# Kernel optimization log

Measured on AMD Instinct MI355X. Metric: run time of the kernel, lower is better.

## Reference

```python
import jax, jax.numpy as jnp
import numpy as np

NEG = -9e15

def _gat_layer(x, adj, W, a_src, a_dst):
    # x: [B,N,Fin], W: [Fin,Fout], a_src/a_dst: [Fout], adj: [N,N]
    h = jnp.einsum('bnf,fo->bno', x, W)                    # [B,N,Fout]
    e_src = jnp.einsum('bno,o->bn', h, a_src)              # [B,N]
    e_dst = jnp.einsum('bno,o->bn', h, a_dst)              # [B,N]
    e = jax.nn.leaky_relu(e_src[:, :, None] + e_dst[:, None, :], 0.2)  # [B,N,N]
    att = jax.nn.softmax(jnp.where(adj > 0, e, NEG), axis=-1)
    return jnp.einsum('bij,bjo->bio', att, h)              # [B,N,Fout]

def setup_inputs() -> dict:
    key = jax.random.key(0)
    ks = jax.random.split(key, 12)
    B, N, Fin = 8, 2048, 128
    H = [128, 128, 64]
    C = 128
    s = lambda *d: 1.0 / np.sqrt(d[0])
    inp = {
        'x':   jax.random.normal(ks[0], (B, N, Fin), jnp.float32),
        'adj': jax.random.normal(ks[1], (N, N), jnp.float32),
        'W1':  jax.random.normal(ks[2], (Fin, H[0]), jnp.float32) * s(Fin),
        'a1s': jax.random.normal(ks[3], (H[0],), jnp.float32) * s(H[0]),
        'a1d': jax.random.normal(ks[4], (H[0],), jnp.float32) * s(H[0]),
        'W2':  jax.random.normal(ks[5], (H[0], H[1]), jnp.float32) * s(H[0]),
        'a2s': jax.random.normal(ks[6], (H[1],), jnp.float32) * s(H[1]),
        'a2d': jax.random.normal(ks[7], (H[1],), jnp.float32) * s(H[1]),
        'W3':  jax.random.normal(ks[8], (H[1], H[2]), jnp.float32) * s(H[1]),
        'a3s': jax.random.normal(ks[9], (H[2],), jnp.float32) * s(H[2]),
        'a3d': jax.random.normal(ks[10], (H[2],), jnp.float32) * s(H[2]),
        'Wlin': jax.random.normal(ks[11], (H[2] * N, C), jnp.float32) * s(H[2] * N),
        'blin': jnp.zeros((C,), jnp.float32),
    }
    return inp

def reference(x, adj, W1, a1s, a1d, W2, a2s, a2d, W3, a3s, a3d, Wlin, blin):
    out = jax.nn.relu(_gat_layer(x, adj, W1, a1s, a1d))
    out = jax.nn.relu(_gat_layer(out, adj, W2, a2s, a2d))
    out = jax.nn.relu(_gat_layer(out, adj, W3, a3s, a3d))
    B = out.shape[0]
    out = out.reshape(B, -1)              # flatten [B, N*H3]
    return out @ Wlin + blin              # [B, num_classes]
```

## Files before the change

### kernel.cpp

```cpp
#include <hip/hip_runtime.h>
#include <stdint.h>


typedef unsigned short u16;
typedef __bf16 bf16x8 __attribute__((ext_vector_type(8)));
typedef float f32x4 __attribute__((ext_vector_type(4)));
typedef float f32x2 __attribute__((ext_vector_type(2)));
typedef u16 u16x8 __attribute__((ext_vector_type(8)));
typedef u16 u16x4 __attribute__((ext_vector_type(4)));

#define LOG2E 1.44269504088896340736f

__device__ __forceinline__ float b2f(u16 u) {
    union { unsigned int i; float f; } v; v.i = ((unsigned int)u) << 16; return v.f;
}
__device__ __forceinline__ u16 f2b(float f) {
    union { float f; unsigned int i; } v; v.f = f;
    unsigned int i = v.i;
    return (u16)((i + 0x7fffu + ((i >> 16) & 1u)) >> 16);
}
__device__ __forceinline__ float fast_exp2(float x) {
#if __has_builtin(__builtin_amdgcn_exp2f)
    return __builtin_amdgcn_exp2f(x);
#else
    return exp2f(x);
#endif
}

union ABfrag { bf16x8 v; u16x8 u; };

__global__ void __launch_bounds__(256) k_mask(const float* __restrict__ adj,
                                              uint32_t* __restrict__ adjm) {
    const int w = threadIdx.x >> 6, lane = threadIdx.x & 63;
    const int row = blockIdx.x * 4 + w;
    const float* ar = adj + (size_t)row * 2048;
    uint32_t* mr = adjm + (size_t)row * 64;
    for (int j0 = 0; j0 < 2048; j0 += 64) {
        unsigned long long m = __ballot(ar[j0 + lane] > 0.f);
        if (lane == 0) {
            mr[(j0 >> 5)] = (uint32_t)m;
            mr[(j0 >> 5) + 1] = (uint32_t)(m >> 32);
        }
    }
}

__global__ void k_prep(const float* __restrict__ W1, const float* __restrict__ W2,
                       const float* __restrict__ W3,
                       const float* __restrict__ a1s, const float* __restrict__ a1d,
                       const float* __restrict__ a2s, const float* __restrict__ a2d,
                       const float* __restrict__ a3s, const float* __restrict__ a3d,
                       u16* __restrict__ Wt1, u16* __restrict__ Wt2, u16* __restrict__ Wt3,
                       float* __restrict__ u1s, float* __restrict__ u1d,
                       float* __restrict__ u2s, float* __restrict__ u2d,
                       float* __restrict__ u3s, float* __restrict__ u3d) {
    if (blockIdx.x == 160) {
        int f = threadIdx.x;
        if (f < 128) {
            float s1 = 0.f, d1 = 0.f, s2 = 0.f, d2 = 0.f, s3 = 0.f, d3 = 0.f;
            for (int o = 0; o < 128; ++o) { float w = W1[f * 128 + o]; s1 += w * a1s[o]; d1 += w * a1d[o]; }
            for (int o = 0; o < 128; ++o) { float w = W2[f * 128 + o]; s2 += w * a2s[o]; d2 += w * a2d[o]; }
            for (int o = 0; o <  64; ++o) { float w = W3[f *  64 + o]; s3 += w * a3s[o]; d3 += w * a3d[o]; }
            u1s[f] = s1 * LOG2E; u1d[f] = d1 * LOG2E;
            u2s[f] = s2 * LOG2E; u2d[f] = d2 * LOG2E;
            u3s[f] = s3 * LOG2E; u3d[f] = d3 * LOG2E;
        }
        return;
    }
    int idx = blockIdx.x * 256 + threadIdx.x;
    if (idx < 16384) {
        int f = idx >> 7, o = idx & 127;
        Wt1[o * 128 + f] = f2b(W1[idx]);
    } else if (idx < 32768) {
        int j = idx - 16384; int f = j >> 7, o = j & 127;
        Wt2[o * 128 + f] = f2b(W2[j]);
    } else if (idx < 40960) {
        int j = idx - 32768; int f = j >> 6, o = j & 63;
        Wt3[o * 128 + f] = f2b(W3[j]);
    }
}

template <int F, bool XF32>
__global__ void __launch_bounds__(256) k_h(const void* __restrict__ xv,
                                           const u16* __restrict__ Wt,
                                           const float* __restrict__ us,
                                           const float* __restrict__ ud,
                                           u16* __restrict__ h_t,
                                           float* __restrict__ esf,
                                           float* __restrict__ edf) {
    constexpr int NTB = F / 32;
    constexpr int TNP = 72;
    __shared__ __align__(16) u16 hl[(F / 2) * TNP];

    const int b = blockIdx.x;
    const int nb2 = blockIdx.y;
    const int nblk = nb2 >> 1, ohalf = nb2 & 1;
    const int tid = threadIdx.x;
    const int w = tid >> 6, lane = tid & 63;
    const int quad = lane >> 4, l15 = lane & 15;
    const int n0w = nblk * 64 + w * 16;
    const int i_a = n0w + l15;

    ABfrag afr[4];
    float ps = 0.f, pd = 0.f;
    if (XF32) {
        const float* xr = (const float*)xv + ((size_t)(b * 2048 + i_a)) * 128;
#pragma unroll
        for (int kk = 0; kk < 4; ++kk) {
            const int o8 = kk * 32 + quad * 8;
            float4 x0 = *reinterpret_cast<const float4*>(xr + o8);
            float4 x1 = *reinterpret_cast<const float4*>(xr + o8 + 4);
            float4 s0 = *reinterpret_cast<const float4*>(us + o8);
            float4 s1 = *reinterpret_cast<const float4*>(us + o8 + 4);
            float4 d0 = *reinterpret_cast<const float4*>(ud + o8);
            float4 d1 = *reinterpret_cast<const float4*>(ud + o8 + 4);
            ps += x0.x * s0.x + x0.y * s0.y + x0.z * s0.z + x0.w * s0.w
                + x1.x * s1.x + x1.y * s1.y + x1.z * s1.z + x1.w * s1.w;
            pd += x0.x * d0.x + x0.y * d0.y + x0.z * d0.z + x0.w * d0.w
                + x1.x * d1.x + x1.y * d1.y + x1.z * d1.z + x1.w * d1.w;
            afr[kk].u[0] = f2b(x0.x); afr[kk].u[1] = f2b(x0.y);
            afr[kk].u[2] = f2b(x0.z); afr[kk].u[3] = f2b(x0.w);
            afr[kk].u[4] = f2b(x1.x); afr[kk].u[5] = f2b(x1.y);
            afr[kk].u[6] = f2b(x1.z); afr[kk].u[7] = f2b(x1.w);
        }
    } else {
        const u16* xr = (const u16*)xv + ((size_t)(b * 2048 + i_a)) * 128;
#pragma unroll
        for (int kk = 0; kk < 4; ++kk) {
            const int o8 = kk * 32 + quad * 8;
            u16x8 xa = *reinterpret_cast<const u16x8*>(xr + o8);
            afr[kk].u = xa;
            float4 s0 = *reinterpret_cast<const float4*>(us + o8);
            float4 s1 = *reinterpret_cast<const float4*>(us + o8 + 4);
            float4 d0 = *reinterpret_cast<const float4*>(ud + o8);
            float4 d1 = *reinterpret_cast<const float4*>(ud + o8 + 4);
            float xf[8];
#pragma unroll
            for (int j = 0; j < 8; ++j) xf[j] = b2f(xa[j]);
            ps += xf[0] * s0.x + xf[1] * s0.y + xf[2] * s0.z + xf[3] * s0.w
                + xf[4] * s1.x + xf[5] * s1.y + xf[6] * s1.z + xf[7] * s1.w;
            pd += xf[0] * d0.x + xf[1] * d0.y + xf[2] * d0.z + xf[3] * d0.w
                + xf[4] * d1.x + xf[5] * d1.y + xf[6] * d1.z + xf[7] * d1.w;
        }
    }
    if (ohalf == 0) {
        ps += __shfl_xor(ps, 16, 64); ps += __shfl_xor(ps, 32, 64);
        pd += __shfl_xor(pd, 16, 64); pd += __shfl_xor(pd, 32, 64);
        if (quad == 0) {
            float2 sv; sv.x = fast_exp2(ps); sv.y = fast_exp2(0.2f * ps);
            *reinterpret_cast<float2*>(esf + (size_t)(b * 2048 + i_a) * 2) = sv;
            edf[(size_t)b * 4096 + i_a]        = fast_exp2(pd);
            edf[(size_t)b * 4096 + 2048 + i_a] = fast_exp2(0.2f * pd);
        }
    }

    f32x4 acc[NTB];
#pragma unroll
    for (int nt = 0; nt < NTB; ++nt) acc[nt] = (f32x4){0.f, 0.f, 0.f, 0.f};
#pragma unroll
    for (int kk = 0; kk < 4; ++kk) {
#pragma unroll
        for (int nt = 0; nt < NTB; ++nt) {
            bf16x8 bfv = *reinterpret_cast<const bf16x8*>(
                Wt + (ohalf * (F / 2) + nt * 16 + l15) * 128 + kk * 32 + quad * 8);
            acc[nt] = __builtin_amdgcn_mfma_f32_16x16x32_bf16(afr[kk].v, bfv, acc[nt], 0, 0, 0);
        }
    }

#pragma unroll
    for (int nt = 0; nt < NTB; ++nt)
#pragma unroll
        for (int r = 0; r < 4; ++r)
            hl[(nt * 16 + l15) * TNP + w * 16 + quad * 4 + r] = f2b(acc[nt][r]);
    __syncthreads();
    if (tid < F) {
        int o_loc = tid >> 1, half32 = tid & 1;
        const u16* src = hl + o_loc * TNP + half32 * 32;
        u16* dst = h_t + ((size_t)(b * F + ohalf * (F / 2) + o_loc)) * 2048
                   + nblk * 64 + half32 * 32;
#pragma unroll
        for (int c = 0; c < 4; ++c)
            *reinterpret_cast<u16x8*>(dst + c * 8) =
                *reinterpret_cast<const u16x8*>(src + c * 8);
    }
}

template <int F, bool OUT_F32>
__global__ void __launch_bounds__(256, 4) k_attn(const float* __restrict__ esf,
                                                 const float* __restrict__ edf,
                                                 const uint32_t* __restrict__ adjm,
                                                 const u16* __restrict__ h_t,
                                                 void* __restrict__ outp) {
    constexpr int FH  = F / 2;
    constexpr int NT2 = FH / 16;
    constexpr int LP_BYTES = 8192 + 8192 + 8192;
    constexpr int CB_BYTES = 4 * 32 * FH * 4 + 512;
    constexpr int LDS_BYTES = (LP_BYTES > CB_BYTES) ? LP_BYTES : CB_BYTES;
    __shared__ __align__(16) char Sraw[LDS_BYTES];
    float* EdL = (float*)Sraw;
    float* FdL = (float*)(Sraw + 8192);
    uint32_t* mL = (uint32_t*)(Sraw + 16384);
    float* part = (float*)Sraw;
    float* denp = (float*)(Sraw + 4 * 32 * FH * 4);

    const int b = blockIdx.x;
    const int i0 = blockIdx.y * 32;
    const int ch = blockIdx.z;
    const int c0 = ch * FH;
    const int tid = threadIdx.x;
    const int w = tid >> 6;
    const int lane = tid & 63;
    const int quad = lane >> 4, l15 = lane & 15;
    const int r0 = l15, r1 = l15 + 16;

    const float2 e0p = *reinterpret_cast<const float2*>(esf + ((size_t)(b * 2048 + i0 + r0)) * 2);
    const float2 e1p = *reinterpret_cast<const float2*>(esf + ((size_t)(b * 2048 + i0 + r1)) * 2);
    const float Es0 = e0p.x, Fs0 = e0p.y, Es1 = e1p.x, Fs1 = e1p.y;
    const u16* hb = h_t + (size_t)b * F * 2048;

    ABfrag onesf;
#pragma unroll
    for (int j = 0; j < 8; ++j) onesf.u[j] = 0x3F80;

    f32x4 acc0[NT2], acc1[NT2];
#pragma unroll
    for (int nt = 0; nt < NT2; ++nt) {
        acc0[nt] = (f32x4){0.f, 0.f, 0.f, 0.f};
        acc1[nt] = (f32x4){0.f, 0.f, 0.f, 0.f};
    }
    f32x4 dn0 = (f32x4){0.f, 0.f, 0.f, 0.f};
    f32x4 dn1 = (f32x4){0.f, 0.f, 0.f, 0.f};

    {
        const float4* eds = (const float4*)(edf + (size_t)b * 4096);
        const float4* fds = (const float4*)(edf + (size_t)b * 4096 + 2048);
        float4* edd = (float4*)EdL;
        float4* fdd = (float4*)FdL;
#pragma unroll
        for (int t = 0; t < 2; ++t) {
            edd[tid + t * 256] = eds[tid + t * 256];
            fdd[tid + t * 256] = fds[tid + t * 256];
        }
        const uint2* msrc = (const uint2*)(adjm + (size_t)i0 * 64);
#pragma unroll
        for (int t = 0; t < 4; ++t) {
            int idx = tid + t * 256;
            int r = idx >> 5, k2 = idx & 31;
            uint2 v = msrc[idx];
            mL[r * 64 + ((2 * k2) ^ r)] = v.x;
            mL[r * 64 + ((2 * k2 + 1) ^ r)] = v.y;
        }
    }
    __syncthreads();

    const int jbase = w * 16;
    auto loadB = [&](int t, ABfrag* bt) {
        const size_t coff = (size_t)((jbase + t) * 32 + quad * 8);
#pragma unroll
        for (int nt = 0; nt < NT2; ++nt)
            bt[nt].u = *reinterpret_cast<const u16x8*>(
                hb + (size_t)(c0 + nt * 16 + l15) * 2048 + coff);
    };

    auto computeTile = [&](int t, ABfrag* bt) {
        const int jt = jbase + t;
        const int j0 = jt * 32;
        const uint32_t mm0 = mL[r0 * 64 + (jt ^ r0)] >> (quad * 8);
        const uint32_t mm1 = mL[r1 * 64 + (jt ^ r1)] >> (quad * 8);
        const f32x2* edp = (const f32x2*)(EdL + j0 + quad * 8);
        const f32x2* fdp = (const f32x2*)(FdL + j0 + quad * 8);

        ABfrag af0, af1;
#pragma unroll
        for (int p = 0; p < 4; ++p) {
            const f32x2 ed = edp[p];
            const f32x2 fd = fdp[p];
            f32x2 a0 = ed * Es0, b0 = fd * Fs0;
            f32x2 a1 = ed * Es1, b1 = fd * Fs1;
            float w0x = fmaxf(a0.x, b0.x), w0y = fmaxf(a0.y, b0.y);
            float w1x = fmaxf(a1.x, b1.x), w1y = fmaxf(a1.y, b1.y);
            const int s0x = ((int)(mm0 << (31 - (p * 2)))) >> 31;
            const int s0y = ((int)(mm0 << (31 - (p * 2 + 1)))) >> 31;
            const int s1x = ((int)(mm1 << (31 - (p * 2)))) >> 31;
            const int s1y = ((int)(mm1 << (31 - (p * 2 + 1)))) >> 31;
            w0x = __uint_as_float(__float_as_uint(w0x) & (uint32_t)s0x);
            w0y = __uint_as_float(__float_as_uint(w0y) & (uint32_t)s0y);
            w1x = __uint_as_float(__float_as_uint(w1x) & (uint32_t)s1x);
            w1y = __uint_as_float(__float_as_uint(w1y) & (uint32_t)s1y);
            af0.v[p * 2]     = (__bf16)w0x;
            af0.v[p * 2 + 1] = (__bf16)w0y;
            af1.v[p * 2]     = (__bf16)w1x;
            af1.v[p * 2 + 1] = (__bf16)w1y;
        }
        __builtin_amdgcn_s_setprio(1);
#pragma unroll
        for (int nt = 0; nt < NT2; ++nt) {
            acc0[nt] = __builtin_amdgcn_mfma_f32_16x16x32_bf16(af0.v, bt[nt].v, acc0[nt], 0, 0, 0);
            acc1[nt] = __builtin_amdgcn_mfma_f32_16x16x32_bf16(af1.v, bt[nt].v, acc1[nt], 0, 0, 0);
        }
        dn0 = __builtin_amdgcn_mfma_f32_16x16x32_bf16(af0.v, onesf.v, dn0, 0, 0, 0);
        dn1 = __builtin_amdgcn_mfma_f32_16x16x32_bf16(af1.v, onesf.v, dn1, 0, 0, 0);
        __builtin_amdgcn_s_setprio(0);
    };

    ABfrag btA[NT2], btB[NT2];
    loadB(0, btA);
    for (int t = 0; t < 16; t += 2) {
        loadB(t + 1, btB);
        computeTile(t, btA);
        if (t + 2 < 16) loadB(t + 2, btA);
        computeTile(t + 1, btB);
    }

    __syncthreads();
    {
        float* pw = part + (size_t)w * 32 * FH;
#pragma unroll
        for (int nt = 0; nt < NT2; ++nt)
#pragma unroll
            for (int r = 0; r < 4; ++r) {
                pw[(quad * 4 + r) * FH + nt * 16 + l15] = acc0[nt][r];
                pw[(16 + quad * 4 + r) * FH + nt * 16 + l15] = acc1[nt][r];
            }
#pragma unroll
        for (int r = 0; r < 4; ++r) {
            denp[w * 32 + quad * 4 + r] = dn0[r];
            denp[w * 32 + 16 + quad * 4 + r] = dn1[r];
        }
    }
    __syncthreads();
    {
        constexpr int C4 = FH / 4;
        for (int idx = tid; idx < 32 * C4; idx += 256) {
            const int row = idx / C4, c4 = idx % C4;
            f32x4 s = *reinterpret_cast<const f32x4*>(&part[row * FH + c4 * 4]);
#pragma unroll
            for (int ww = 1; ww < 4; ++ww)
                s += *reinterpret_cast<const f32x4*>(&part[(ww * 32 + row) * FH + c4 * 4]);
            const float den = denp[row] + denp[32 + row] + denp[64 + row] + denp[96 + row];
            const float dinv = 1.0f / fmaxf(den, 1e-30f);
            if (OUT_F32) {
                float4 o;
                o.x = fmaxf(s[0] * dinv, 0.f); o.y = fmaxf(s[1] * dinv, 0.f);
                o.z = fmaxf(s[2] * dinv, 0.f); o.w = fmaxf(s[3] * dinv, 0.f);
                *reinterpret_cast<float4*>((float*)outp +
                    ((size_t)(b * 2048 + i0 + row)) * F + c0 + c4 * 4) = o;
            } else {
                u16x4 o;
                o[0] = f2b(fmaxf(s[0] * dinv, 0.f)); o[1] = f2b(fmaxf(s[1] * dinv, 0.f));
                o[2] = f2b(fmaxf(s[2] * dinv, 0.f)); o[3] = f2b(fmaxf(s[3] * dinv, 0.f));
                *reinterpret_cast<u16x4*>((u16*)outp +
                    ((size_t)(b * 2048 + i0 + row)) * F + c0 + c4 * 4) = o;
            }
        }
    }
}

__global__ void __launch_bounds__(256) k_lin(const float* __restrict__ o3,
                                             const float* __restrict__ Wlin,
                                             float* __restrict__ pbuf) {
    __shared__ float xc[8][256];
    __shared__ float red[8][8][128];
    const int tid = threadIdx.x;
    const int k0 = blockIdx.x * 256;
    for (int idx = tid; idx < 2048; idx += 256) {
        int bb = idx >> 8, kk = idx & 255;
        xc[bb][kk] = o3[(size_t)bb * 131072 + k0 + kk];
    }
    __syncthreads();
    const int o4 = tid & 31;
    const int kb = tid >> 5;
    f32x4 acc[8];
#pragma unroll
    for (int bb = 0; bb < 8; ++bb) acc[bb] = (f32x4){0.f, 0.f, 0.f, 0.f};
    const float* wp = Wlin + (size_t)(k0 + kb * 32) * 128 + o4 * 4;
#pragma unroll 4
    for (int k = 0; k < 32; ++k) {
        f32x4 wv = *reinterpret_cast<const f32x4*>(wp + (size_t)k * 128);
#pragma unroll
        for (int bb = 0; bb < 8; ++bb) acc[bb] += wv * xc[bb][kb * 32 + k];
    }
#pragma unroll
    for (int bb = 0; bb < 8; ++bb)
        *reinterpret_cast<f32x4*>(&red[kb][bb][o4 * 4]) = acc[bb];
    __syncthreads();
    const int f = tid * 4;
    const int bb = f >> 7, o = f & 127;
    f32x4 s = (f32x4){0.f, 0.f, 0.f, 0.f};
#pragma unroll
    for (int k2 = 0; k2 < 8; ++k2) s += *reinterpret_cast<const f32x4*>(&red[k2][bb][o]);
    *reinterpret_cast<f32x4*>(&pbuf[(size_t)blockIdx.x * 1024 + f]) = s;
}

__global__ void __launch_bounds__(256) k_bias(const float* __restrict__ pbuf,
                                              const float* __restrict__ blin,
                                              float* __restrict__ out) {
    __shared__ float red[256];
    const int tid = threadIdx.x;
    const int p16 = tid >> 4;
    const int fo = tid & 15;
    const int f0 = blockIdx.x * 16;
    float s = 0.f;
#pragma unroll 4
    for (int p = p16; p < 512; p += 16)
        s += pbuf[(size_t)p * 1024 + f0 + fo];
    red[tid] = s;
    __syncthreads();
    if (tid < 16) {
        float t = 0.f;
#pragma unroll
        for (int k = 0; k < 16; ++k) t += red[k * 16 + tid];
        out[f0 + tid] = t + blin[(f0 + tid) & 127];
    }
}

extern "C" void kernel_launch(void* const* d_in, const int* in_sizes, int n_in,
                              void* d_out, int out_size, void* d_ws, size_t ws_size,
                              hipStream_t stream) {
    (void)in_sizes; (void)n_in; (void)out_size;
    const float* x    = (const float*)d_in[0];
    const float* adj  = (const float*)d_in[1];
    const float* W1   = (const float*)d_in[2];
    const float* a1s  = (const float*)d_in[3];
    const float* a1d  = (const float*)d_in[4];
    const float* W2   = (const float*)d_in[5];
    const float* a2s  = (const float*)d_in[6];
    const float* a2d  = (const float*)d_in[7];
    const float* W3   = (const float*)d_in[8];
    const float* a3s  = (const float*)d_in[9];
    const float* a3d  = (const float*)d_in[10];
    const float* Wlin = (const float*)d_in[11];
    const float* blin = (const float*)d_in[12];

    char* ws = (char*)d_ws;
    u16*   h_t = (u16*)ws;
    size_t off = (size_t)4 << 20;
    float* esf = (float*)(ws + off); off += 131072;
    float* edf = (float*)(ws + off); off += 131072;
    u16*   Wt1 = (u16*)(ws + off);   off += 32768;
    u16*   Wt2 = (u16*)(ws + off);   off += 32768;
    u16*   Wt3 = (u16*)(ws + off);   off += 16384;
    float* u1s = (float*)(ws + off); off += 512;
    float* u1d = (float*)(ws + off); off += 512;
    float* u2s = (float*)(ws + off); off += 512;
    float* u2d = (float*)(ws + off); off += 512;
    float* u3s = (float*)(ws + off); off += 512;
    float* u3d = (float*)(ws + off); off += 512;
    uint32_t* adjm = (uint32_t*)(ws + off); off += 524288;
    float* pbuf = (float*)(ws + off); off += (size_t)512 * 1024 * 4;
    u16* actA;
    if (ws_size >= off + ((size_t)4 << 20)) {
        actA = (u16*)(ws + off);
    } else {
        actA = (u16*)d_in[0];
    }
    float* o3 = (float*)actA;

    dim3 ga(8, 64, 2);
    dim3 gh(8, 64);
    k_mask<<<512, 256, 0, stream>>>(adj, adjm);
    k_prep<<<161, 256, 0, stream>>>(W1, W2, W3, a1s, a1d, a2s, a2d, a3s, a3d,
                                    Wt1, Wt2, Wt3, u1s, u1d, u2s, u2d, u3s, u3d);

    k_h<128, true ><<<gh, 256, 0, stream>>>((const void*)x, Wt1, u1s, u1d, h_t, esf, edf);
    k_attn<128, false><<<ga, 256, 0, stream>>>(esf, edf, adjm, h_t, (void*)actA);

    k_h<128, false><<<gh, 256, 0, stream>>>((const void*)actA, Wt2, u2s, u2d, h_t, esf, edf);
    k_attn<128, false><<<ga, 256, 0, stream>>>(esf, edf, adjm, h_t, (void*)actA);

    k_h<64, false><<<gh, 256, 0, stream>>>((const void*)actA, Wt3, u3s, u3d, h_t, esf, edf);
    k_attn<64, true ><<<ga, 256, 0, stream>>>(esf, edf, adjm, h_t, (void*)o3);

    k_lin<<<512, 256, 0, stream>>>(o3, Wlin, pbuf);
    k_bias<<<64, 256, 0, stream>>>(pbuf, blin, (float*)d_out);
}
```

Baseline: 276.6 us.

## Tile h into contiguous 32-column blocks and triple-buffer B fragment loads

k_h now writes h in a tiled layout [b][jtile][F][32], so each 32-node tile's features for all output channels are contiguous. The B fragments in k_attn then come from a compact block instead of rows strided 4 KB apart. The attention loop moves from double to triple buffering with a full unroll, which prefetches two tiles ahead, and the Ed/Fd LDS reads are widened to 128-bit loads. The cost is higher register pressure from the third buffer set, which could hurt occupancy under the (256,4) launch bounds.

```diff
diff --git a/kernel.cpp b/kernel.cpp
--- a/kernel.cpp
+++ b/kernel.cpp
@@ -84,7 +84,7 @@
                                            const u16* __restrict__ Wt,
                                            const float* __restrict__ us,
                                            const float* __restrict__ ud,
-                                           u16* __restrict__ h_t,
+                                           u16* __restrict__ h2,
                                            float* __restrict__ esf,
                                            float* __restrict__ edf) {
     constexpr int NTB = F / 32;
@@ -175,8 +175,8 @@
     if (tid < F) {
         int o_loc = tid >> 1, half32 = tid & 1;
         const u16* src = hl + o_loc * TNP + half32 * 32;
-        u16* dst = h_t + ((size_t)(b * F + ohalf * (F / 2) + o_loc)) * 2048
-                   + nblk * 64 + half32 * 32;
+        const int jt = nblk * 2 + half32;
+        u16* dst = h2 + (((size_t)(b * 64 + jt)) * F + ohalf * (F / 2) + o_loc) * 32;
 #pragma unroll
         for (int c = 0; c < 4; ++c)
             *reinterpret_cast<u16x8*>(dst + c * 8) =
@@ -188,7 +188,7 @@
 __global__ void __launch_bounds__(256, 4) k_attn(const float* __restrict__ esf,
                                                  const float* __restrict__ edf,
                                                  const uint32_t* __restrict__ adjm,
-                                                 const u16* __restrict__ h_t,
+                                                 const u16* __restrict__ h2,
                                                  void* __restrict__ outp) {
     constexpr int FH  = F / 2;
     constexpr int NT2 = FH / 16;
@@ -215,7 +215,7 @@
     const float2 e0p = *reinterpret_cast<const float2*>(esf + ((size_t)(b * 2048 + i0 + r0)) * 2);
     const float2 e1p = *reinterpret_cast<const float2*>(esf + ((size_t)(b * 2048 + i0 + r1)) * 2);
     const float Es0 = e0p.x, Fs0 = e0p.y, Es1 = e1p.x, Fs1 = e1p.y;
-    const u16* hb = h_t + (size_t)b * F * 2048;
+    const u16* hb2 = h2 + (size_t)b * 64 * F * 32;
 
     ABfrag onesf;
 #pragma unroll
@@ -253,31 +253,37 @@
     __syncthreads();
 
     const int jbase = w * 16;
-    auto loadB = [&](int t, ABfrag* bt) {
-        const size_t coff = (size_t)((jbase + t) * 32 + quad * 8);
+    auto loadB = [&](int t, ABfrag* dst) {
+        const u16* src = hb2 + (((size_t)(jbase + t)) * F + c0) * 32;
 #pragma unroll
         for (int nt = 0; nt < NT2; ++nt)
-            bt[nt].u = *reinterpret_cast<const u16x8*>(
-                hb + (size_t)(c0 + nt * 16 + l15) * 2048 + coff);
+            dst[nt].u = *reinterpret_cast<const u16x8*>(
+                src + (nt * 16 + l15) * 32 + quad * 8);
     };
 
-    auto computeTile = [&](int t, ABfrag* bt) {
+    auto computeTile = [&](int t, ABfrag* btp) {
         const int jt = jbase + t;
         const int j0 = jt * 32;
         const uint32_t mm0 = mL[r0 * 64 + (jt ^ r0)] >> (quad * 8);
         const uint32_t mm1 = mL[r1 * 64 + (jt ^ r1)] >> (quad * 8);
-        const f32x2* edp = (const f32x2*)(EdL + j0 + quad * 8);
-        const f32x2* fdp = (const f32x2*)(FdL + j0 + quad * 8);
+        const f32x4 ed01 = *reinterpret_cast<const f32x4*>(EdL + j0 + quad * 8);
+        const f32x4 ed23 = *reinterpret_cast<const f32x4*>(EdL + j0 + quad * 8 + 4);
+        const f32x4 fd01 = *reinterpret_cast<const f32x4*>(FdL + j0 + quad * 8);
+        const f32x4 fd23 = *reinterpret_cast<const f32x4*>(FdL + j0 + quad * 8 + 4);
+        const float edv[8] = {ed01[0], ed01[1], ed01[2], ed01[3],
+                              ed23[0], ed23[1], ed23[2], ed23[3]};
+        const float fdv[8] = {fd01[0], fd01[1], fd01[2], fd01[3],
+                              fd23[0], fd23[1], fd23[2], fd23[3]};
 
         ABfrag af0, af1;
 #pragma unroll
         for (int p = 0; p < 4; ++p) {
-            const f32x2 ed = edp[p];
-            const f32x2 fd = fdp[p];
-            f32x2 a0 = ed * Es0, b0 = fd * Fs0;
-            f32x2 a1 = ed * Es1, b1 = fd * Fs1;
-            float w0x = fmaxf(a0.x, b0.x), w0y = fmaxf(a0.y, b0.y);
-            float w1x = fmaxf(a1.x, b1.x), w1y = fmaxf(a1.y, b1.y);
+            const float ex = edv[p * 2], ey = edv[p * 2 + 1];
+            const float fx = fdv[p * 2], fy = fdv[p * 2 + 1];
+            float w0x = fmaxf(ex * Es0, fx * Fs0);
+            float w0y = fmaxf(ey * Es0, fy * Fs0);
+            float w1x = fmaxf(ex * Es1, fx * Fs1);
+            float w1y = fmaxf(ey * Es1, fy * Fs1);
             const int s0x = ((int)(mm0 << (31 - (p * 2)))) >> 31;
             const int s0y = ((int)(mm0 << (31 - (p * 2 + 1)))) >> 31;
             const int s1x = ((int)(mm1 << (31 - (p * 2)))) >> 31;
@@ -294,21 +300,21 @@
         __builtin_amdgcn_s_setprio(1);
 #pragma unroll
         for (int nt = 0; nt < NT2; ++nt) {
-            acc0[nt] = __builtin_amdgcn_mfma_f32_16x16x32_bf16(af0.v, bt[nt].v, acc0[nt], 0, 0, 0);
-            acc1[nt] = __builtin_amdgcn_mfma_f32_16x16x32_bf16(af1.v, bt[nt].v, acc1[nt], 0, 0, 0);
+            acc0[nt] = __builtin_amdgcn_mfma_f32_16x16x32_bf16(af0.v, btp[nt].v, acc0[nt], 0, 0, 0);
+            acc1[nt] = __builtin_amdgcn_mfma_f32_16x16x32_bf16(af1.v, btp[nt].v, acc1[nt], 0, 0, 0);
         }
         dn0 = __builtin_amdgcn_mfma_f32_16x16x32_bf16(af0.v, onesf.v, dn0, 0, 0, 0);
         dn1 = __builtin_amdgcn_mfma_f32_16x16x32_bf16(af1.v, onesf.v, dn1, 0, 0, 0);
         __builtin_amdgcn_s_setprio(0);
     };
 
-    ABfrag btA[NT2], btB[NT2];
-    loadB(0, btA);
-    for (int t = 0; t < 16; t += 2) {
-        loadB(t + 1, btB);
-        computeTile(t, btA);
-        if (t + 2 < 16) loadB(t + 2, btA);
-        computeTile(t + 1, btB);
+    ABfrag bt[3][NT2];
+    loadB(0, bt[0]);
+    loadB(1, bt[1]);
+#pragma unroll
+    for (int t = 0; t < 16; ++t) {
+        if (t < 14) loadB(t + 2, bt[(t + 2) % 3]);
+        computeTile(t, bt[t % 3]);
     }
 
     __syncthreads();
@@ -432,7 +438,7 @@
     const float* blin = (const float*)d_in[12];
 
     char* ws = (char*)d_ws;
-    u16*   h_t = (u16*)ws;
+    u16*   h2  = (u16*)ws;
     size_t off = (size_t)4 << 20;
     float* esf = (float*)(ws + off); off += 131072;
     float* edf = (float*)(ws + off); off += 131072;
@@ -461,14 +467,14 @@
     k_prep<<<161, 256, 0, stream>>>(W1, W2, W3, a1s, a1d, a2s, a2d, a3s, a3d,
                                     Wt1, Wt2, Wt3, u1s, u1d, u2s, u2d, u3s, u3d);
 
-    k_h<128, true ><<<gh, 256, 0, stream>>>((const void*)x, Wt1, u1s, u1d, h_t, esf, edf);
-    k_attn<128, false><<<ga, 256, 0, stream>>>(esf, edf, adjm, h_t, (void*)actA);
-
-    k_h<128, false><<<gh, 256, 0, stream>>>((const void*)actA, Wt2, u2s, u2d, h_t, esf, edf);
-    k_attn<128, false><<<ga, 256, 0, stream>>>(esf, edf, adjm, h_t, (void*)actA);
-
-    k_h<64, false><<<gh, 256, 0, stream>>>((const void*)actA, Wt3, u3s, u3d, h_t, esf, edf);
-    k_attn<64, true ><<<ga, 256, 0, stream>>>(esf, edf, adjm, h_t, (void*)o3);
+    k_h<128, true ><<<gh, 256, 0, stream>>>((const void*)x, Wt1, u1s, u1d, h2, esf, edf);
+    k_attn<128, false><<<ga, 256, 0, stream>>>(esf, edf, adjm, h2, (void*)actA);
+
+    k_h<128, false><<<gh, 256, 0, stream>>>((const void*)actA, Wt2, u2s, u2d, h2, esf, edf);
+    k_attn<128, false><<<ga, 256, 0, stream>>>(esf, edf, adjm, h2, (void*)actA);
+
+    k_h<64, false><<<gh, 256, 0, stream>>>((const void*)actA, Wt3, u3s, u3d, h2, esf, edf);
+    k_attn<64, true ><<<ga, 256, 0, stream>>>(esf, edf, adjm, h2, (void*)o3);
 
     k_lin<<<512, 256, 0, stream>>>(o3, Wlin, pbuf);
     k_bias<<<64, 256, 0, stream>>>(pbuf, blin, (float*)d_out);
```

Result: no change. 280.2 us (+1.3%).
